# Performance work log

Measured on AMD Instinct MI355X. Metric: run time of the kernel, lower is better.

The kernel has to match this reference:

```python
import jax, jax.numpy as jnp
import numpy as np

N_NODES = 50000
N_GRAPHS = 512
HID = 128
IN = 128
SLOPE = 0.2  # LeakyReLU negative slope (PyG default)


def _gatv2(x, src, dst, Wl, bl, Wr, br, att, bias, n):
    # PyG GATv2Conv, 1 head: xl used for source/messages, xr for targets
    xl = x @ Wl + bl          # [N, H]
    xr = x @ Wr + br          # [N, H]
    # per-edge score: att . LeakyReLU(xl[j] + xr[i])
    e = jax.nn.leaky_relu(xl[src] + xr[dst], SLOPE) @ att  # [E]
    # softmax grouped by destination node (self loops guarantee nonempty groups)
    m = jax.ops.segment_max(e, dst, num_segments=n)
    p = jnp.exp(e - m[dst])
    s = jax.ops.segment_sum(p, dst, num_segments=n)
    alpha = p / s[dst]                                      # [E]
    out = jax.ops.segment_sum(alpha[:, None] * xl[src], dst, num_segments=n)
    return out + bias


def setup_inputs() -> dict:
    key = jax.random.key(0)
    ks = jax.random.split(key, 24)
    x = jax.random.normal(ks[0], (N_NODES, IN), jnp.float32)
    edge_index = jax.random.randint(ks[1], (2, 1600000), 0, N_NODES, jnp.int64)
    batch = jnp.sort(jax.random.randint(ks[2], (N_NODES,), 0, N_GRAPHS, jnp.int64))

    def lin(k, fi, fo):
        k1, k2 = jax.random.split(k)
        sc = 1.0 / np.sqrt(fi)
        return (jax.random.uniform(k1, (fi, fo), jnp.float32, -sc, sc),
                jax.random.uniform(k2, (fo,), jnp.float32, -sc, sc))

    d = {"x": x, "edge_index": edge_index, "batch": batch}
    dims = [(IN, HID), (HID, HID), (HID, HID)]
    for i, (fi, fo) in enumerate(dims, 1):
        Wl, bl = lin(ks[3 * i], fi, fo)
        Wr, br = lin(ks[3 * i + 1], fi, fo)
        d[f"Wl{i}"], d[f"bl{i}"] = Wl, bl
        d[f"Wr{i}"], d[f"br{i}"] = Wr, br
        d[f"att{i}"] = jax.random.normal(ks[3 * i + 2], (fo,), jnp.float32) / np.sqrt(fo)
        d[f"bias{i}"] = jnp.zeros((fo,), jnp.float32)
    d["W4"], d["b4"] = lin(ks[15], HID, 128)
    d["W5"], d["b5"] = lin(ks[16], 128, 64)
    d["W6"], d["b6"] = lin(ks[17], 64, 2)
    return d


def reference(x, edge_index, batch,
              Wl1, bl1, Wr1, br1, att1, bias1,
              Wl2, bl2, Wr2, br2, att2, bias2,
              Wl3, bl3, Wr3, br3, att3, bias3,
              W4, b4, W5, b5, W6, b6):
    n = x.shape[0]
    loop = jnp.arange(n, dtype=edge_index.dtype)
    src = jnp.concatenate([edge_index[0], loop])  # add_self_loops=True
    dst = jnp.concatenate([edge_index[1], loop])

    h = jax.nn.relu(_gatv2(x, src, dst, Wl1, bl1, Wr1, br1, att1, bias1, n))
    h = jax.nn.relu(_gatv2(h, src, dst, Wl2, bl2, Wr2, br2, att2, bias2, n))
    h = _gatv2(h, src, dst, Wl3, bl3, Wr3, br3, att3, bias3, n)

    # global_mean_pool over graph ids
    sums = jax.ops.segment_sum(h, batch, num_segments=N_GRAPHS)
    cnts = jax.ops.segment_sum(jnp.ones((n,), h.dtype), batch, num_segments=N_GRAPHS)
    g = sums / jnp.maximum(cnts, 1.0)[:, None]

    # dropout is identity in eval mode; MLP head
    g = jax.nn.sigmoid(g @ W4 + b4)
    g = jax.nn.sigmoid(g @ W5 + b5)
    return g @ W6 + b6
```

## Files before the change

kernel.cpp:

```cpp
#include <hip/hip_runtime.h>
#include <math.h>

#define BK_SHIFT 7
#define BK_NODES 128

typedef _Float16 h2 __attribute__((ext_vector_type(2)));
typedef _Float16 f16x8 __attribute__((ext_vector_type(8)));
typedef float f32x4 __attribute__((ext_vector_type(4)));

__device__ __forceinline__ h2 u2h(unsigned u){ return __builtin_bit_cast(h2, u); }

__device__ __forceinline__ int dev_lower_bound(const int* __restrict__ a, int n, int v){
  int lo = 0, hi = n;
  while (lo < hi){ int mid = (lo + hi) >> 1; if (a[mid] < v) lo = mid + 1; else hi = mid; }
  return lo;
}

__global__ __launch_bounds__(256) void p1_prep_kernel(
    const int* __restrict__ edst, int* __restrict__ bktTotal, int nE, int K,
    const float* __restrict__ W0, const float* __restrict__ W1,
    const float* __restrict__ W2, const float* __restrict__ W3,
    const float* __restrict__ W4m, const float* __restrict__ W5m,
    unsigned short* __restrict__ Wt16)
{
  __shared__ int cnt[512];
  if (blockIdx.x < 48){
    const float* Ws[6] = {W0, W1, W2, W3, W4m, W5m};
    const int mat = blockIdx.x >> 3;
    const int chunk = blockIdx.x & 7;
    const float* W = Ws[mat];
    unsigned short* o = Wt16 + mat * 16384;
    #pragma unroll
    for (int e = 0; e < 8; ++e){
      int i = chunk * 2048 + e * 256 + threadIdx.x;
      int k = i >> 7, col = i & 127;
      _Float16 h = (_Float16)W[i];
      o[col * 128 + k] = __builtin_bit_cast(unsigned short, h);
    }
    return;
  }
  const int bx = blockIdx.x - 48;
  for (int k = threadIdx.x; k < K; k += 256) cnt[k] = 0;
  __syncthreads();
  int i = (bx * 256 + threadIdx.x) * 8;
  if (i + 7 < nE){
    int4 a = *(const int4*)(edst + i);
    int4 b = *(const int4*)(edst + i + 4);
    atomicAdd(&cnt[a.x >> BK_SHIFT], 1); atomicAdd(&cnt[a.y >> BK_SHIFT], 1);
    atomicAdd(&cnt[a.z >> BK_SHIFT], 1); atomicAdd(&cnt[a.w >> BK_SHIFT], 1);
    atomicAdd(&cnt[b.x >> BK_SHIFT], 1); atomicAdd(&cnt[b.y >> BK_SHIFT], 1);
    atomicAdd(&cnt[b.z >> BK_SHIFT], 1); atomicAdd(&cnt[b.w >> BK_SHIFT], 1);
  } else {
    for (int j = i; j < nE; ++j) atomicAdd(&cnt[edst[j] >> BK_SHIFT], 1);
  }
  __syncthreads();
  for (int k = threadIdx.x; k < K; k += 256)
    if (cnt[k]) atomicAdd(&bktTotal[k], cnt[k]);
}

__global__ __launch_bounds__(512) void p2_scan(const int* __restrict__ bktTotal,
    int* __restrict__ bktBase, int* __restrict__ bktCur,
    int* __restrict__ row_off, int K, int n, int nE){
  __shared__ int sh[512];
  int t = threadIdx.x;
  int v = (t < K) ? bktTotal[t] : 0;
  sh[t] = v;
  __syncthreads();
  for (int off = 1; off < 512; off <<= 1){
    int u = (t >= off) ? sh[t - off] : 0;
    __syncthreads();
    sh[t] += u;
    __syncthreads();
  }
  if (t < K){
    int excl = sh[t] - v;
    bktBase[t] = excl;
    bktCur[t]  = excl;
  }
  if (t == 0){
    bktBase[K] = nE;
    row_off[n] = nE + n;
  }
}

__global__ __launch_bounds__(256) void p3_partition(const int* __restrict__ esrc,
    const int* __restrict__ edst, int* __restrict__ bktCur,
    unsigned* __restrict__ ebuf, int nE, int K){
  __shared__ int cnt[512];
  __shared__ int base[512];
  for (int k = threadIdx.x; k < K; k += 256) cnt[k] = 0;
  __syncthreads();
  const int i0 = (blockIdx.x * 256 + threadIdx.x) * 8;
  const int i1 = min(i0 + 8, nE);
  int bkt[8];
  unsigned pk[8];
  int cnt_local = i1 - i0;
  for (int j = 0; j < cnt_local; ++j){
    int sv = esrc[i0 + j];
    int dv = edst[i0 + j];
    bkt[j] = dv >> BK_SHIFT;
    pk[j] = ((unsigned)sv << BK_SHIFT) | (unsigned)(dv & (BK_NODES - 1));
    atomicAdd(&cnt[bkt[j]], 1);
  }
  __syncthreads();
  for (int k = threadIdx.x; k < K; k += 256){
    int c = cnt[k];
    base[k] = c ? atomicAdd(&bktCur[k], c) : 0;
  }
  __syncthreads();
  for (int k = threadIdx.x; k < K; k += 256) cnt[k] = 0;
  __syncthreads();
  for (int j = 0; j < cnt_local; ++j){
    int r = atomicAdd(&cnt[bkt[j]], 1);
    ebuf[base[bkt[j]] + r] = pk[j];
  }
}

__global__ __launch_bounds__(256) void p4_build(const unsigned* __restrict__ ebuf,
    const int* __restrict__ bktBase, int* __restrict__ row_off,
    int* __restrict__ csr_src, int* __restrict__ dbins, int n){
  const int b = blockIdx.x;
  const int node0 = b << BK_SHIFT;
  const int nNodes = min(BK_NODES, n - node0);
  const int tid = threadIdx.x;
  __shared__ int ldeg[BK_NODES];
  __shared__ int lcur[BK_NODES];
  __shared__ int sc[BK_NODES];
  __shared__ int dh[256];
  const int e0 = bktBase[b];
  const int e1 = bktBase[b + 1];
  if (tid < BK_NODES) ldeg[tid] = 0;
  dh[tid] = 0;
  __syncthreads();
  for (int i = e0 + tid; i < e1; i += 256)
    atomicAdd(&ldeg[ebuf[i] & (BK_NODES - 1)], 1);
  __syncthreads();
  if (tid < BK_NODES) sc[tid] = (tid < nNodes) ? (ldeg[tid] + 1) : 0;
  __syncthreads();
  for (int off = 1; off < BK_NODES; off <<= 1){
    int u = 0;
    if (tid < BK_NODES && tid >= off) u = sc[tid - off];
    __syncthreads();
    if (tid < BK_NODES) sc[tid] += u;
    __syncthreads();
  }
  if (tid < nNodes){
    const int csr0 = e0 + node0;
    int ro = csr0 + sc[tid] - (ldeg[tid] + 1);
    row_off[node0 + tid] = ro;
    lcur[tid] = ro;
    atomicAdd(&dh[255 - min(ldeg[tid] + 1, 255)], 1);
  }
  __syncthreads();
  for (int i = e0 + tid; i < e1; i += 256){
    unsigned e = ebuf[i];
    int p = atomicAdd(&lcur[e & (BK_NODES - 1)], 1);
    csr_src[p] = (int)(e >> BK_SHIFT);
  }
  __syncthreads();
  if (tid < nNodes)
    csr_src[lcur[tid]] = node0 + tid;
  if (dh[tid]) atomicAdd(&dbins[tid], dh[tid]);
}

__global__ __launch_bounds__(256) void deg_scan(const int* __restrict__ dbins,
    int* __restrict__ dcur){
  __shared__ int sh[256];
  int t = threadIdx.x;
  int v = dbins[t];
  sh[t] = v;
  __syncthreads();
  for (int off = 1; off < 256; off <<= 1){
    int u = (t >= off) ? sh[t - off] : 0;
    __syncthreads();
    sh[t] += u;
    __syncthreads();
  }
  dcur[t] = sh[t] - v;
}

__global__ __launch_bounds__(256) void deg_scatter(const int* __restrict__ row_off,
    int* __restrict__ dcur, int* __restrict__ order, int n){
  __shared__ int cnt[256];
  __shared__ int base[256];
  cnt[threadIdx.x] = 0;
  __syncthreads();
  int i = blockIdx.x * 256 + threadIdx.x;
  int bin = 0, r = 0;
  if (i < n){
    int deg = row_off[i + 1] - row_off[i];
    bin = 255 - min(deg, 255);
    r = atomicAdd(&cnt[bin], 1);
  }
  __syncthreads();
  base[threadIdx.x] = cnt[threadIdx.x] ? atomicAdd(&dcur[threadIdx.x], cnt[threadIdx.x]) : 0;
  __syncthreads();
  if (i < n) order[base[bin] + r] = i;
}

template<bool F16IN>
__global__ __launch_bounds__(256) void gemm_mfma_kernel(
    const void* __restrict__ Xv,
    const unsigned short* __restrict__ WtL,
    const float* __restrict__ bl, const float* __restrict__ br,
    unsigned short* __restrict__ xl16, unsigned short* __restrict__ xr16, int n)
{
  const int mat = blockIdx.y;
  const unsigned short* Wt = WtL + mat * 16384;
  const float* bias = mat ? br : bl;
  unsigned short* out = mat ? xr16 : xl16;
  const int w   = threadIdx.x >> 6;
  const int l   = threadIdx.x & 63;
  const int l15 = l & 15;
  const int kq  = l >> 4;
  const int rowbase = blockIdx.x * 128 + w * 32;

  f16x8 a[2][4];
  #pragma unroll
  for (int rt = 0; rt < 2; ++rt){
    const int r = rowbase + rt * 16 + l15;
    const bool ok = r < n;
    const int rc = min(r, n - 1);
    #pragma unroll
    for (int ks = 0; ks < 4; ++ks){
      if (F16IN){
        const unsigned short* src = (const unsigned short*)Xv + (size_t)rc * 128 + kq * 8 + ks * 32;
        f16x8 v = ok ? *(const f16x8*)src : (f16x8){0,0,0,0,0,0,0,0};
        a[rt][ks] = v;
      } else {
        const float* src = (const float*)Xv + (size_t)rc * 128 + kq * 8 + ks * 32;
        float4 f0 = ok ? *(const float4*)(src)     : make_float4(0.f,0.f,0.f,0.f);
        float4 f1 = ok ? *(const float4*)(src + 4) : make_float4(0.f,0.f,0.f,0.f);
        f16x8 v;
        v[0] = (_Float16)f0.x; v[1] = (_Float16)f0.y;
        v[2] = (_Float16)f0.z; v[3] = (_Float16)f0.w;
        v[4] = (_Float16)f1.x; v[5] = (_Float16)f1.y;
        v[6] = (_Float16)f1.z; v[7] = (_Float16)f1.w;
        a[rt][ks] = v;
      }
    }
  }

  f32x4 acc[2][8];
  #pragma unroll
  for (int rt = 0; rt < 2; ++rt)
    #pragma unroll
    for (int ct = 0; ct < 8; ++ct)
      acc[rt][ct] = (f32x4){0.f, 0.f, 0.f, 0.f};

  #pragma unroll
  for (int ks = 0; ks < 4; ++ks){
    #pragma unroll
    for (int ct = 0; ct < 8; ++ct){
      f16x8 b = *(const f16x8*)(Wt + (size_t)(ct * 16 + l15) * 128 + ks * 32 + kq * 8);
      acc[0][ct] = __builtin_amdgcn_mfma_f32_16x16x32_f16(a[0][ks], b, acc[0][ct], 0, 0, 0);
      acc[1][ct] = __builtin_amdgcn_mfma_f32_16x16x32_f16(a[1][ks], b, acc[1][ct], 0, 0, 0);
    }
  }

  #pragma unroll
  for (int ct = 0; ct < 8; ++ct){
    const float bv = bias[ct * 16 + l15];
    #pragma unroll
    for (int rt = 0; rt < 2; ++rt){
      #pragma unroll
      for (int rg = 0; rg < 4; ++rg){
        const int r = rowbase + rt * 16 + kq * 4 + rg;
        if (r < n){
          _Float16 h = (_Float16)(acc[rt][ct][rg] + bv);
          out[(size_t)r * 128 + ct * 16 + l15] = __builtin_bit_cast(unsigned short, h);
        }
      }
    }
  }
}

__global__ __launch_bounds__(256) void edge_attn_kernel(
    const unsigned short* __restrict__ xl16, const unsigned short* __restrict__ xr16,
    const int* __restrict__ row_off, const int* __restrict__ csr_src,
    const int* __restrict__ order,
    const float* __restrict__ att, const float* __restrict__ bias,
    unsigned short* __restrict__ out16, int n, int do_relu)
{
  const int gid = (blockIdx.x * blockDim.x + threadIdx.x) >> 4;
  const int node = order[min(gid, n - 1)];
  const int lane16 = threadIdx.x & 15;
  const int f8 = lane16 * 8;

  const uint4 xru = *(const uint4*)(xr16 + (size_t)node * 128 + f8);
  const h2 xr0 = u2h(xru.x), xr1 = u2h(xru.y), xr2 = u2h(xru.z), xr3 = u2h(xru.w);
  const float4 aA = *(const float4*)(att + f8);
  const float4 aB = *(const float4*)(att + f8 + 4);
  const h2 at0 = {(_Float16)aA.x, (_Float16)aA.y};
  const h2 at1 = {(_Float16)aA.z, (_Float16)aA.w};
  const h2 at2 = {(_Float16)aB.x, (_Float16)aB.y};
  const h2 at3 = {(_Float16)aB.z, (_Float16)aB.w};
  const h2 k02 = {(_Float16)0.2f, (_Float16)0.2f};

  const int base = row_off[node];
  const int deg  = row_off[node + 1] - base;
  int dmax = max(deg, __shfl_xor(deg, 16));
  dmax = max(dmax, __shfl_xor(dmax, 32));

  auto part = [&](uint4 xp) -> float {
    h2 u0 = u2h(xp.x) + xr0;
    h2 u1 = u2h(xp.y) + xr1;
    h2 u2 = u2h(xp.z) + xr2;
    h2 u3 = u2h(xp.w) + xr3;
    u0 = __builtin_elementwise_max(u0, u0 * k02);
    u1 = __builtin_elementwise_max(u1, u1 * k02);
    u2 = __builtin_elementwise_max(u2, u2 * k02);
    u3 = __builtin_elementwise_max(u3, u3 * k02);
    float ps = __builtin_amdgcn_fdot2(u0, at0, 0.f, false);
    ps = __builtin_amdgcn_fdot2(u1, at1, ps, false);
    ps = __builtin_amdgcn_fdot2(u2, at2, ps, false);
    ps = __builtin_amdgcn_fdot2(u3, at3, ps, false);
    return ps;
  };

  uint4 xp = *(const uint4*)(xl16 + (size_t)csr_src[base] * 128 + f8);
  float p = part(xp);
  p += __shfl_xor(p, 1); p += __shfl_xor(p, 2);
  p += __shfl_xor(p, 4); p += __shfl_xor(p, 8);
  float m = p, Mrun = p, s = 1.f;
  float a0 = (float)u2h(xp.x).x, a1 = (float)u2h(xp.x).y;
  float a2 = (float)u2h(xp.y).x, a3 = (float)u2h(xp.y).y;
  float a4 = (float)u2h(xp.z).x, a5 = (float)u2h(xp.z).y;
  float a6 = (float)u2h(xp.w).x, a7 = (float)u2h(xp.w).y;

  for (int it = 1; it < dmax; it += 4){
    const int c0 = min(it,     deg - 1);
    const int c1 = min(it + 1, deg - 1);
    const int c2 = min(it + 2, deg - 1);
    const int c3 = min(it + 3, deg - 1);
    const int s0 = csr_src[base + c0];
    const int s1 = csr_src[base + c1];
    const int s2 = csr_src[base + c2];
    const int s3 = csr_src[base + c3];
    const uint4 xA = *(const uint4*)(xl16 + (size_t)s0 * 128 + f8);
    const uint4 xB = *(const uint4*)(xl16 + (size_t)s1 * 128 + f8);
    const uint4 xC = *(const uint4*)(xl16 + (size_t)s2 * 128 + f8);
    const uint4 xD = *(const uint4*)(xl16 + (size_t)s3 * 128 + f8);
    float pA = part(xA), pB = part(xB), pC = part(xC), pD = part(xD);
    #pragma unroll
    for (int off = 1; off < 16; off <<= 1){
      pA += __shfl_xor(pA, off);
      pB += __shfl_xor(pB, off);
      pC += __shfl_xor(pC, off);
      pD += __shfl_xor(pD, off);
    }
    const bool vA = it < deg, vB = it + 1 < deg, vC = it + 2 < deg, vD = it + 3 < deg;
    float fA = vA ? pA : -3.0e38f;
    float fB = vB ? pB : -3.0e38f;
    float fC = vC ? pC : -3.0e38f;
    float fD = vD ? pD : -3.0e38f;
    Mrun = fmaxf(Mrun, fmaxf(fmaxf(fA, fB), fmaxf(fC, fD)));
    if (__any(Mrun > m + 8.f)){
      float sc = __expf(m - Mrun);
      s *= sc;
      a0 *= sc; a1 *= sc; a2 *= sc; a3 *= sc;
      a4 *= sc; a5 *= sc; a6 *= sc; a7 *= sc;
      m = Mrun;
    }
    float qA = vA ? __expf(pA - m) : 0.f;
    float qB = vB ? __expf(pB - m) : 0.f;
    float qC = vC ? __expf(pC - m) : 0.f;
    float qD = vD ? __expf(pD - m) : 0.f;
    s += (qA + qB) + (qC + qD);
    h2 w;
    w = u2h(xA.x); a0 = fmaf(qA, (float)w.x, a0); a1 = fmaf(qA, (float)w.y, a1);
    w = u2h(xA.y); a2 = fmaf(qA, (float)w.x, a2); a3 = fmaf(qA, (float)w.y, a3);
    w = u2h(xA.z); a4 = fmaf(qA, (float)w.x, a4); a5 = fmaf(qA, (float)w.y, a5);
    w = u2h(xA.w); a6 = fmaf(qA, (float)w.x, a6); a7 = fmaf(qA, (float)w.y, a7);
    w = u2h(xB.x); a0 = fmaf(qB, (float)w.x, a0); a1 = fmaf(qB, (float)w.y, a1);
    w = u2h(xB.y); a2 = fmaf(qB, (float)w.x, a2); a3 = fmaf(qB, (float)w.y, a3);
    w = u2h(xB.z); a4 = fmaf(qB, (float)w.x, a4); a5 = fmaf(qB, (float)w.y, a5);
    w = u2h(xB.w); a6 = fmaf(qB, (float)w.x, a6); a7 = fmaf(qB, (float)w.y, a7);
    w = u2h(xC.x); a0 = fmaf(qC, (float)w.x, a0); a1 = fmaf(qC, (float)w.y, a1);
    w = u2h(xC.y); a2 = fmaf(qC, (float)w.x, a2); a3 = fmaf(qC, (float)w.y, a3);
    w = u2h(xC.z); a4 = fmaf(qC, (float)w.x, a4); a5 = fmaf(qC, (float)w.y, a5);
    w = u2h(xC.w); a6 = fmaf(qC, (float)w.x, a6); a7 = fmaf(qC, (float)w.y, a7);
    w = u2h(xD.x); a0 = fmaf(qD, (float)w.x, a0); a1 = fmaf(qD, (float)w.y, a1);
    w = u2h(xD.y); a2 = fmaf(qD, (float)w.x, a2); a3 = fmaf(qD, (float)w.y, a3);
    w = u2h(xD.z); a4 = fmaf(qD, (float)w.x, a4); a5 = fmaf(qD, (float)w.y, a5);
    w = u2h(xD.w); a6 = fmaf(qD, (float)w.x, a6); a7 = fmaf(qD, (float)w.y, a7);
  }

  if (gid < n){
    const float inv = 1.0f / s;
    const float4 bA = *(const float4*)(bias + f8);
    const float4 bB = *(const float4*)(bias + f8 + 4);
    float o0 = fmaf(a0, inv, bA.x), o1 = fmaf(a1, inv, bA.y);
    float o2 = fmaf(a2, inv, bA.z), o3 = fmaf(a3, inv, bA.w);
    float o4 = fmaf(a4, inv, bB.x), o5 = fmaf(a5, inv, bB.y);
    float o6 = fmaf(a6, inv, bB.z), o7 = fmaf(a7, inv, bB.w);
    if (do_relu){
      o0 = fmaxf(o0, 0.f); o1 = fmaxf(o1, 0.f); o2 = fmaxf(o2, 0.f); o3 = fmaxf(o3, 0.f);
      o4 = fmaxf(o4, 0.f); o5 = fmaxf(o5, 0.f); o6 = fmaxf(o6, 0.f); o7 = fmaxf(o7, 0.f);
    }
    ushort4 wlo, whi;
    wlo.x = __builtin_bit_cast(unsigned short, (_Float16)o0);
    wlo.y = __builtin_bit_cast(unsigned short, (_Float16)o1);
    wlo.z = __builtin_bit_cast(unsigned short, (_Float16)o2);
    wlo.w = __builtin_bit_cast(unsigned short, (_Float16)o3);
    whi.x = __builtin_bit_cast(unsigned short, (_Float16)o4);
    whi.y = __builtin_bit_cast(unsigned short, (_Float16)o5);
    whi.z = __builtin_bit_cast(unsigned short, (_Float16)o6);
    whi.w = __builtin_bit_cast(unsigned short, (_Float16)o7);
    *(ushort4*)(out16 + (size_t)node * 128 + f8)     = wlo;
    *(ushort4*)(out16 + (size_t)node * 128 + f8 + 4) = whi;
  }
}

__global__ __launch_bounds__(128) void pool_mlp_kernel(
    const unsigned short* __restrict__ h, const int* __restrict__ batch, int n,
    const float* __restrict__ W4, const float* __restrict__ b4,
    const float* __restrict__ W5, const float* __restrict__ b5,
    const float* __restrict__ W6, const float* __restrict__ b6,
    float* __restrict__ out)
{
  int g = blockIdx.x;
  int t = threadIdx.x;
  __shared__ float gf[128];
  __shared__ float h1[128];
  __shared__ float h2s[64];
  int lo = dev_lower_bound(batch, n, g);
  int hi = dev_lower_bound(batch, n, g + 1);
  float ssum = 0.f;
  for (int i = lo; i < hi; ++i){
    _Float16 hv = __builtin_bit_cast(_Float16, h[(size_t)i * 128 + t]);
    ssum += (float)hv;
  }
  float cnt = (float)(hi - lo);
  gf[t] = ssum / fmaxf(cnt, 1.0f);
  __syncthreads();
  float a = b4[t];
  for (int k = 0; k < 128; ++k) a = fmaf(gf[k], W4[k * 128 + t], a);
  h1[t] = 1.0f / (1.0f + __expf(-a));
  __syncthreads();
  if (t < 64){
    float a5 = b5[t];
    for (int k = 0; k < 128; ++k) a5 = fmaf(h1[k], W5[k * 64 + t], a5);
    h2s[t] = 1.0f / (1.0f + __expf(-a5));
  }
  __syncthreads();
  if (t < 2){
    float a6 = b6[t];
    for (int k = 0; k < 64; ++k) a6 = fmaf(h2s[k], W6[k * 2 + t], a6);
    out[g * 2 + t] = a6;
  }
}

extern "C" void kernel_launch(void* const* d_in, const int* in_sizes, int n_in,
                              void* d_out, int out_size, void* d_ws, size_t ws_size,
                              hipStream_t stream)
{
  const float* x          = (const float*)d_in[0];
  const int*   edge_index = (const int*)d_in[1];
  const int*   batch      = (const int*)d_in[2];
  const int n  = in_sizes[0] / 128;
  const int nE = in_sizes[1] / 2;
  const int* esrc = edge_index;
  const int* edst = edge_index + nE;
  const int n_graphs = out_size / 2;
  const int K = (n + BK_NODES - 1) >> BK_SHIFT;

  const float *Wl[3], *bl[3], *Wr[3], *br[3], *att[3], *bias[3];
  for (int l = 0; l < 3; ++l){
    Wl[l]   = (const float*)d_in[3 + 6 * l + 0];
    bl[l]   = (const float*)d_in[3 + 6 * l + 1];
    Wr[l]   = (const float*)d_in[3 + 6 * l + 2];
    br[l]   = (const float*)d_in[3 + 6 * l + 3];
    att[l]  = (const float*)d_in[3 + 6 * l + 4];
    bias[l] = (const float*)d_in[3 + 6 * l + 5];
  }
  const float* W4 = (const float*)d_in[21]; const float* b4 = (const float*)d_in[22];
  const float* W5 = (const float*)d_in[23]; const float* b5 = (const float*)d_in[24];
  const float* W6 = (const float*)d_in[25]; const float* b6 = (const float*)d_in[26];

  char* ws = (char*)d_ws;
  size_t off = 0;
  auto alloc = [&](size_t bytes) -> void* {
    void* p = ws + off;
    off = (off + bytes + 255) & ~(size_t)255;
    return p;
  };
  int*   row_off  = (int*)  alloc((size_t)(n + 1) * sizeof(int));
  int*   meta     = (int*)  alloc(2049 * sizeof(int));
  int*   bktTotal = meta;
  int*   bktBase  = meta + 512;
  int*   bktCur   = meta + 1025;
  int*   dbins    = meta + 1537;
  int*   dcur     = meta + 1793;
  int*   order    = (int*)  alloc((size_t)n * sizeof(int));
  int*   csr_src  = (int*)  alloc((size_t)(nE + n) * sizeof(int));
  unsigned* ebuf  = (unsigned*)alloc((size_t)nE * sizeof(unsigned));
  unsigned short* xlb16 = (unsigned short*)alloc((size_t)n * 128 * sizeof(unsigned short));
  unsigned short* xrb16 = (unsigned short*)alloc((size_t)n * 128 * sizeof(unsigned short));
  unsigned short* Wt16  = (unsigned short*)alloc(6 * 16384 * sizeof(unsigned short));
  unsigned short* hC16  = (unsigned short*)alloc((size_t)n * 128 * sizeof(unsigned short));
  (void)ws_size; (void)n_in;

  hipMemsetAsync(meta, 0, 2049 * sizeof(int), stream);

  const int eblocks = (nE + 2048 - 1) / 2048;
  p1_prep_kernel<<<eblocks + 48, 256, 0, stream>>>(edst, bktTotal, nE, K,
      Wl[0], Wr[0], Wl[1], Wr[1], Wl[2], Wr[2], Wt16);
  p2_scan<<<1, 512, 0, stream>>>(bktTotal, bktBase, bktCur, row_off, K, n, nE);
  p3_partition<<<eblocks, 256, 0, stream>>>(esrc, edst, bktCur, ebuf, nE, K);
  p4_build<<<K, 256, 0, stream>>>(ebuf, bktBase, row_off, csr_src, dbins, n);

  deg_scan<<<1, 256, 0, stream>>>(dbins, dcur);
  deg_scatter<<<(n + 255) / 256, 256, 0, stream>>>(row_off, dcur, order, n);

  const int gemm_tiles = (n + 127) / 128;
  const int attn_blocks = (int)(((size_t)n * 16 + 255) / 256);

  gemm_mfma_kernel<false><<<dim3(gemm_tiles, 2), 256, 0, stream>>>(x, Wt16 + 0 * 32768,
                                                            bl[0], br[0], xlb16, xrb16, n);
  edge_attn_kernel<<<attn_blocks, 256, 0, stream>>>(xlb16, xrb16, row_off, csr_src, order,
                                                    att[0], bias[0], hC16, n, 1);
  gemm_mfma_kernel<true><<<dim3(gemm_tiles, 2), 256, 0, stream>>>(hC16, Wt16 + 1 * 32768,
                                                            bl[1], br[1], xlb16, xrb16, n);
  edge_attn_kernel<<<attn_blocks, 256, 0, stream>>>(xlb16, xrb16, row_off, csr_src, order,
                                                    att[1], bias[1], hC16, n, 1);
  gemm_mfma_kernel<true><<<dim3(gemm_tiles, 2), 256, 0, stream>>>(hC16, Wt16 + 2 * 32768,
                                                            bl[2], br[2], xlb16, xrb16, n);
  edge_attn_kernel<<<attn_blocks, 256, 0, stream>>>(xlb16, xrb16, row_off, csr_src, order,
                                                    att[2], bias[2], hC16, n, 0);

  pool_mlp_kernel<<<n_graphs, 128, 0, stream>>>(hC16, batch, n, W4, b4, W5, b5, W6, b6,
                                                (float*)d_out);
}
```

Measured before the change: 419.6 us.

## Fold bucket scan into partition/build kernels and accumulate attention in packed fp16

Removes the single-block p2_scan launch: every p3_partition block now recomputes the bucket prefix scan locally, and each p4_build block sums the bucket totals before it to get its edge range. row_off[n] is written in deg_scan instead. Separately, the edge attention aggregation now accumulates weighted neighbour features in packed half2 registers with fp16 weights instead of fp32 FMAs, halving the arithmetic but risking precision loss and overflow in long softmax sums. Together these cut one launch and ALU work in the hot gather loop, at the cost of redundant scan work per block.

```diff
diff --git a/kernel.cpp b/kernel.cpp
--- a/kernel.cpp
+++ b/kernel.cpp
@@ -58,39 +58,30 @@
     if (cnt[k]) atomicAdd(&bktTotal[k], cnt[k]);
 }
 
-__global__ __launch_bounds__(512) void p2_scan(const int* __restrict__ bktTotal,
-    int* __restrict__ bktBase, int* __restrict__ bktCur,
-    int* __restrict__ row_off, int K, int n, int nE){
+__global__ __launch_bounds__(256) void p3_partition(const int* __restrict__ esrc,
+    const int* __restrict__ edst, const int* __restrict__ bktTotal,
+    int* __restrict__ bktCur, unsigned* __restrict__ ebuf, int nE, int K){
   __shared__ int sh[512];
-  int t = threadIdx.x;
-  int v = (t < K) ? bktTotal[t] : 0;
-  sh[t] = v;
-  __syncthreads();
-  for (int off = 1; off < 512; off <<= 1){
-    int u = (t >= off) ? sh[t - off] : 0;
-    __syncthreads();
-    sh[t] += u;
-    __syncthreads();
-  }
-  if (t < K){
-    int excl = sh[t] - v;
-    bktBase[t] = excl;
-    bktCur[t]  = excl;
-  }
-  if (t == 0){
-    bktBase[K] = nE;
-    row_off[n] = nE + n;
-  }
-}
-
-__global__ __launch_bounds__(256) void p3_partition(const int* __restrict__ esrc,
-    const int* __restrict__ edst, int* __restrict__ bktCur,
-    unsigned* __restrict__ ebuf, int nE, int K){
   __shared__ int cnt[512];
   __shared__ int base[512];
-  for (int k = threadIdx.x; k < K; k += 256) cnt[k] = 0;
-  __syncthreads();
-  const int i0 = (blockIdx.x * 256 + threadIdx.x) * 8;
+  const int t = threadIdx.x;
+  const int tot0 = (t < K) ? bktTotal[t] : 0;
+  const int tot1 = (t + 256 < K) ? bktTotal[t + 256] : 0;
+  sh[t] = tot0; sh[t + 256] = tot1;
+  __syncthreads();
+  for (int off = 1; off < 512; off <<= 1){
+    int v0 = (t >= off) ? sh[t - off] : 0;
+    int v1 = (t + 256 >= off) ? sh[t + 256 - off] : 0;
+    __syncthreads();
+    sh[t] += v0; sh[t + 256] += v1;
+    __syncthreads();
+  }
+  base[t] = sh[t] - tot0;
+  base[t + 256] = sh[t + 256] - tot1;
+  cnt[t] = 0; cnt[t + 256] = 0;
+  __syncthreads();
+
+  const int i0 = (blockIdx.x * 256 + t) * 8;
   const int i1 = min(i0 + 8, nE);
   int bkt[8];
   unsigned pk[8];
@@ -103,21 +94,21 @@
     atomicAdd(&cnt[bkt[j]], 1);
   }
   __syncthreads();
-  for (int k = threadIdx.x; k < K; k += 256){
+  for (int k = t; k < K; k += 256){
     int c = cnt[k];
-    base[k] = c ? atomicAdd(&bktCur[k], c) : 0;
-  }
-  __syncthreads();
-  for (int k = threadIdx.x; k < K; k += 256) cnt[k] = 0;
+    sh[k] = c ? (base[k] + atomicAdd(&bktCur[k], c)) : 0;
+  }
+  __syncthreads();
+  for (int k = t; k < K; k += 256) cnt[k] = 0;
   __syncthreads();
   for (int j = 0; j < cnt_local; ++j){
     int r = atomicAdd(&cnt[bkt[j]], 1);
-    ebuf[base[bkt[j]] + r] = pk[j];
+    ebuf[sh[bkt[j]] + r] = pk[j];
   }
 }
 
 __global__ __launch_bounds__(256) void p4_build(const unsigned* __restrict__ ebuf,
-    const int* __restrict__ bktBase, int* __restrict__ row_off,
+    const int* __restrict__ bktTotal, int* __restrict__ row_off,
     int* __restrict__ csr_src, int* __restrict__ dbins, int n){
   const int b = blockIdx.x;
   const int node0 = b << BK_SHIFT;
@@ -127,8 +118,18 @@
   __shared__ int lcur[BK_NODES];
   __shared__ int sc[BK_NODES];
   __shared__ int dh[256];
-  const int e0 = bktBase[b];
-  const int e1 = bktBase[b + 1];
+  __shared__ int red[256];
+  int partial = 0;
+  for (int k = tid; k < b; k += 256) partial += bktTotal[k];
+  red[tid] = partial;
+  __syncthreads();
+  for (int off = 128; off > 0; off >>= 1){
+    if (tid < off) red[tid] += red[tid + off];
+    __syncthreads();
+  }
+  const int e0 = red[0];
+  const int e1 = e0 + bktTotal[b];
+  __syncthreads();
   if (tid < BK_NODES) ldeg[tid] = 0;
   dh[tid] = 0;
   __syncthreads();
@@ -164,7 +165,7 @@
 }
 
 __global__ __launch_bounds__(256) void deg_scan(const int* __restrict__ dbins,
-    int* __restrict__ dcur){
+    int* __restrict__ dcur, int* __restrict__ row_off, int n, int nE){
   __shared__ int sh[256];
   int t = threadIdx.x;
   int v = dbins[t];
@@ -177,6 +178,7 @@
     __syncthreads();
   }
   dcur[t] = sh[t] - v;
+  if (t == 0) row_off[n] = nE + n;
 }
 
 __global__ __launch_bounds__(256) void deg_scatter(const int* __restrict__ row_off,
@@ -323,10 +325,7 @@
   p += __shfl_xor(p, 1); p += __shfl_xor(p, 2);
   p += __shfl_xor(p, 4); p += __shfl_xor(p, 8);
   float m = p, Mrun = p, s = 1.f;
-  float a0 = (float)u2h(xp.x).x, a1 = (float)u2h(xp.x).y;
-  float a2 = (float)u2h(xp.y).x, a3 = (float)u2h(xp.y).y;
-  float a4 = (float)u2h(xp.z).x, a5 = (float)u2h(xp.z).y;
-  float a6 = (float)u2h(xp.w).x, a7 = (float)u2h(xp.w).y;
+  h2 A0 = u2h(xp.x), A1 = u2h(xp.y), A2 = u2h(xp.z), A3 = u2h(xp.w);
 
   for (int it = 1; it < dmax; it += 4){
     const int c0 = min(it,     deg - 1);
@@ -358,8 +357,9 @@
     if (__any(Mrun > m + 8.f)){
       float sc = __expf(m - Mrun);
       s *= sc;
-      a0 *= sc; a1 *= sc; a2 *= sc; a3 *= sc;
-      a4 *= sc; a5 *= sc; a6 *= sc; a7 *= sc;
+      _Float16 hs = (_Float16)sc;
+      h2 scv = {hs, hs};
+      A0 *= scv; A1 *= scv; A2 *= scv; A3 *= scv;
       m = Mrun;
     }
     float qA = vA ? __expf(pA - m) : 0.f;
@@ -367,33 +367,26 @@
     float qC = vC ? __expf(pC - m) : 0.f;
     float qD = vD ? __expf(pD - m) : 0.f;
     s += (qA + qB) + (qC + qD);
-    h2 w;
-    w = u2h(xA.x); a0 = fmaf(qA, (float)w.x, a0); a1 = fmaf(qA, (float)w.y, a1);
-    w = u2h(xA.y); a2 = fmaf(qA, (float)w.x, a2); a3 = fmaf(qA, (float)w.y, a3);
-    w = u2h(xA.z); a4 = fmaf(qA, (float)w.x, a4); a5 = fmaf(qA, (float)w.y, a5);
-    w = u2h(xA.w); a6 = fmaf(qA, (float)w.x, a6); a7 = fmaf(qA, (float)w.y, a7);
-    w = u2h(xB.x); a0 = fmaf(qB, (float)w.x, a0); a1 = fmaf(qB, (float)w.y, a1);
-    w = u2h(xB.y); a2 = fmaf(qB, (float)w.x, a2); a3 = fmaf(qB, (float)w.y, a3);
-    w = u2h(xB.z); a4 = fmaf(qB, (float)w.x, a4); a5 = fmaf(qB, (float)w.y, a5);
-    w = u2h(xB.w); a6 = fmaf(qB, (float)w.x, a6); a7 = fmaf(qB, (float)w.y, a7);
-    w = u2h(xC.x); a0 = fmaf(qC, (float)w.x, a0); a1 = fmaf(qC, (float)w.y, a1);
-    w = u2h(xC.y); a2 = fmaf(qC, (float)w.x, a2); a3 = fmaf(qC, (float)w.y, a3);
-    w = u2h(xC.z); a4 = fmaf(qC, (float)w.x, a4); a5 = fmaf(qC, (float)w.y, a5);
-    w = u2h(xC.w); a6 = fmaf(qC, (float)w.x, a6); a7 = fmaf(qC, (float)w.y, a7);
-    w = u2h(xD.x); a0 = fmaf(qD, (float)w.x, a0); a1 = fmaf(qD, (float)w.y, a1);
-    w = u2h(xD.y); a2 = fmaf(qD, (float)w.x, a2); a3 = fmaf(qD, (float)w.y, a3);
-    w = u2h(xD.z); a4 = fmaf(qD, (float)w.x, a4); a5 = fmaf(qD, (float)w.y, a5);
-    w = u2h(xD.w); a6 = fmaf(qD, (float)w.x, a6); a7 = fmaf(qD, (float)w.y, a7);
+    _Float16 ha = (_Float16)qA, hb = (_Float16)qB, hc = (_Float16)qC, hd = (_Float16)qD;
+    h2 qa = {ha, ha}, qb = {hb, hb}, qc = {hc, hc}, qd = {hd, hd};
+    A0 += u2h(xA.x) * qa; A1 += u2h(xA.y) * qa;
+    A2 += u2h(xA.z) * qa; A3 += u2h(xA.w) * qa;
+    A0 += u2h(xB.x) * qb; A1 += u2h(xB.y) * qb;
+    A2 += u2h(xB.z) * qb; A3 += u2h(xB.w) * qb;
+    A0 += u2h(xC.x) * qc; A1 += u2h(xC.y) * qc;
+    A2 += u2h(xC.z) * qc; A3 += u2h(xC.w) * qc;
+    A0 += u2h(xD.x) * qd; A1 += u2h(xD.y) * qd;
+    A2 += u2h(xD.z) * qd; A3 += u2h(xD.w) * qd;
   }
 
   if (gid < n){
     const float inv = 1.0f / s;
     const float4 bA = *(const float4*)(bias + f8);
     const float4 bB = *(const float4*)(bias + f8 + 4);
-    float o0 = fmaf(a0, inv, bA.x), o1 = fmaf(a1, inv, bA.y);
-    float o2 = fmaf(a2, inv, bA.z), o3 = fmaf(a3, inv, bA.w);
-    float o4 = fmaf(a4, inv, bB.x), o5 = fmaf(a5, inv, bB.y);
-    float o6 = fmaf(a6, inv, bB.z), o7 = fmaf(a7, inv, bB.w);
+    float o0 = fmaf((float)A0.x, inv, bA.x), o1 = fmaf((float)A0.y, inv, bA.y);
+    float o2 = fmaf((float)A1.x, inv, bA.z), o3 = fmaf((float)A1.y, inv, bA.w);
+    float o4 = fmaf((float)A2.x, inv, bB.x), o5 = fmaf((float)A2.y, inv, bB.y);
+    float o6 = fmaf((float)A3.x, inv, bB.z), o7 = fmaf((float)A3.y, inv, bB.w);
     if (do_relu){
       o0 = fmaxf(o0, 0.f); o1 = fmaxf(o1, 0.f); o2 = fmaxf(o2, 0.f); o3 = fmaxf(o3, 0.f);
       o4 = fmaxf(o4, 0.f); o5 = fmaxf(o5, 0.f); o6 = fmaxf(o6, 0.f); o7 = fmaxf(o7, 0.f);
@@ -486,12 +479,11 @@
     return p;
   };
   int*   row_off  = (int*)  alloc((size_t)(n + 1) * sizeof(int));
-  int*   meta     = (int*)  alloc(2049 * sizeof(int));
+  int*   meta     = (int*)  alloc(1536 * sizeof(int));
   int*   bktTotal = meta;
-  int*   bktBase  = meta + 512;
-  int*   bktCur   = meta + 1025;
-  int*   dbins    = meta + 1537;
-  int*   dcur     = meta + 1793;
+  int*   bktCur   = meta + 512;
+  int*   dbins    = meta + 1024;
+  int*   dcur     = meta + 1280;
   int*   order    = (int*)  alloc((size_t)n * sizeof(int));
   int*   csr_src  = (int*)  alloc((size_t)(nE + n) * sizeof(int));
   unsigned* ebuf  = (unsigned*)alloc((size_t)nE * sizeof(unsigned));
@@ -501,16 +493,15 @@
   unsigned short* hC16  = (unsigned short*)alloc((size_t)n * 128 * sizeof(unsigned short));
   (void)ws_size; (void)n_in;
 
-  hipMemsetAsync(meta, 0, 2049 * sizeof(int), stream);
+  hipMemsetAsync(meta, 0, 1536 * sizeof(int), stream);
 
   const int eblocks = (nE + 2048 - 1) / 2048;
   p1_prep_kernel<<<eblocks + 48, 256, 0, stream>>>(edst, bktTotal, nE, K,
       Wl[0], Wr[0], Wl[1], Wr[1], Wl[2], Wr[2], Wt16);
-  p2_scan<<<1, 512, 0, stream>>>(bktTotal, bktBase, bktCur, row_off, K, n, nE);
-  p3_partition<<<eblocks, 256, 0, stream>>>(esrc, edst, bktCur, ebuf, nE, K);
-  p4_build<<<K, 256, 0, stream>>>(ebuf, bktBase, row_off, csr_src, dbins, n);
-
-  deg_scan<<<1, 256, 0, stream>>>(dbins, dcur);
+  p3_partition<<<eblocks, 256, 0, stream>>>(esrc, edst, bktTotal, bktCur, ebuf, nE, K);
+  p4_build<<<K, 256, 0, stream>>>(ebuf, bktTotal, row_off, csr_src, dbins, n);
+
+  deg_scan<<<1, 256, 0, stream>>>(dbins, dcur, row_off, n, nE);
   deg_scatter<<<(n + 255) / 256, 256, 0, stream>>>(row_off, dcur, order, n);
 
   const int gemm_tiles = (n + 127) / 128;
```

New measurement: 410.3 us. 2.2% less time.
